# Kernel optimization log

Hardware: AMD Instinct MI355X
Metric: run time of the kernel (lower is better)

## Reference

```python
import jax, jax.numpy as jnp
import numpy as np

N_CLASSES = 91  # classes 0..90; class 0 (background) is excluded from the mean


def setup_inputs() -> dict:
    key = jax.random.key(0)
    k1, k2 = jax.random.split(key)
    B, H, W = 64, 512, 512
    # label maps with integer class ids in [0, 91); `inputs` stored as float32
    # to mirror the original (compared elementwise against integer i)
    inputs = jax.random.randint(k1, (B, H, W), 0, N_CLASSES).astype(jnp.float32)
    targets = jax.random.randint(k2, (B, H, W), 0, N_CLASSES).astype(jnp.int32)
    return {"inputs": inputs, "targets": targets, "smooth": 1}


def reference(inputs, targets, smooth):
    # Single-pass histogram formulation of the original per-class loop:
    #   intersection_i = #{p : inputs[p]==i and targets[p]==i}
    #   total_i        = #{inputs==i} + #{targets==i}
    #   union_i        = total_i - intersection_i
    n = N_CLASSES
    inp = inputs.reshape(-1).astype(jnp.int32)
    tgt = targets.reshape(-1).astype(jnp.int32)
    cnt_in = jnp.bincount(inp, length=n).astype(jnp.float32)
    cnt_tg = jnp.bincount(tgt, length=n).astype(jnp.float32)
    # positions where prediction == target contribute to that class's intersection;
    # mismatches are routed to a dummy bin n and dropped
    inter = jnp.bincount(jnp.where(inp == tgt, inp, n), length=n + 1)[:n].astype(jnp.float32)
    union = cnt_in + cnt_tg - inter
    smooth_f = jnp.float32(smooth)
    iou = (inter[1:] + smooth_f) / (union[1:] + smooth_f)  # classes 1..n-1
    return jnp.sum(iou) / (n - 1)
```

## Files before the change

### kernel.cpp

```cpp
#include <hip/hip_runtime.h>

#define NCLS 91
#define NPPAD 8284
#define NHIST (3 * NCLS)
#define BS 256
#define NBLK 1024
#define U 8
#define NCHUNK 2

__global__ __launch_bounds__(BS) void miou_hist(const float* __restrict__ inp,
                                                const int* __restrict__ tgt,
                                                unsigned int* __restrict__ ws,
                                                int n4) {
    __shared__ unsigned int ph[NPPAD];
    uint4* z = (uint4*)ph;
    for (int i = threadIdx.x; i < NPPAD / 4; i += BS) z[i] = make_uint4(0u, 0u, 0u, 0u);
    __syncthreads();

    const float4* in4 = (const float4*)inp;
    const int4* tg4 = (const int4*)tgt;
    const int stride = NBLK * BS;
    const int i0 = blockIdx.x * BS + threadIdx.x;

    if (i0 + (NCHUNK * U - 1) * stride < n4) {
        #pragma unroll
        for (int c = 0; c < NCHUNK; ++c) {
            const int base = i0 + c * U * stride;
            float4 f[U];
            int4 t[U];
            #pragma unroll
            for (int u = 0; u < U; ++u) {
                f[u] = in4[base + u * stride];
                t[u] = tg4[base + u * stride];
            }
            __builtin_amdgcn_sched_barrier(0);
            #pragma unroll
            for (int u = 0; u < U; ++u) {
                atomicAdd(&ph[(int)f[u].x * NCLS + t[u].x], 1u);
                atomicAdd(&ph[(int)f[u].y * NCLS + t[u].y], 1u);
                atomicAdd(&ph[(int)f[u].z * NCLS + t[u].z], 1u);
                atomicAdd(&ph[(int)f[u].w * NCLS + t[u].w], 1u);
            }
        }
    } else {
        for (int i = i0; i < n4; i += stride) {
            float4 f = in4[i];
            int4 t = tg4[i];
            atomicAdd(&ph[(int)f.x * NCLS + t.x], 1u);
            atomicAdd(&ph[(int)f.y * NCLS + t.y], 1u);
            atomicAdd(&ph[(int)f.z * NCLS + t.z], 1u);
            atomicAdd(&ph[(int)f.w * NCLS + t.w], 1u);
        }
    }
    __syncthreads();

    int t = threadIdx.x;
    if (t < NCLS) {
        const unsigned int* p = ph + t * NCLS;
        unsigned int s0 = 0, s1 = 0, s2 = 0, s3 = 0;
        int k = 0;
        for (; k + 3 < NCLS; k += 4) { s0 += p[k]; s1 += p[k+1]; s2 += p[k+2]; s3 += p[k+3]; }
        for (; k < NCLS; ++k) s0 += p[k];
        unsigned int s = s0 + s1 + s2 + s3;
        if (s) atomicAdd(&ws[t], s);
        unsigned int d = p[t];
        if (d) atomicAdd(&ws[2 * NCLS + t], d);
    } else if (t >= 128 && t < 128 + NCLS) {
        int c = t - 128;
        unsigned int s0 = 0, s1 = 0, s2 = 0, s3 = 0;
        int a = 0;
        for (; a + 3 < NCLS; a += 4) {
            s0 += ph[a * NCLS + c];
            s1 += ph[(a + 1) * NCLS + c];
            s2 += ph[(a + 2) * NCLS + c];
            s3 += ph[(a + 3) * NCLS + c];
        }
        for (; a < NCLS; ++a) s0 += ph[a * NCLS + c];
        unsigned int s = s0 + s1 + s2 + s3;
        if (s) atomicAdd(&ws[NCLS + c], s);
    }
}

__global__ void miou_tail(const float* __restrict__ inp, const int* __restrict__ tgt,
                          unsigned int* __restrict__ ws, int e0, int n) {
    int i = e0 + blockIdx.x * 256 + threadIdx.x;
    if (i < n) {
        int a = (int)inp[i];
        int t = tgt[i];
        atomicAdd(&ws[a], 1u);
        atomicAdd(&ws[NCLS + t], 1u);
        if (a == t) atomicAdd(&ws[2 * NCLS + a], 1u);
    }
}

__global__ void miou_finalize(const unsigned int* __restrict__ ws,
                              const int* __restrict__ smooth_p,
                              float* __restrict__ out) {
    int lane = threadIdx.x;
    float s = (float)(*smooth_p);
    float acc = 0.f;
    for (int c = 1 + lane; c < NCLS; c += 64) {
        float ci = (float)ws[c];
        float ct = (float)ws[NCLS + c];
        float it = (float)ws[2 * NCLS + c];
        float un = ci + ct - it;
        acc += (it + s) / (un + s);
    }
    #pragma unroll
    for (int off = 32; off; off >>= 1) acc += __shfl_down(acc, off);
    if (lane == 0) out[0] = acc / (float)(NCLS - 1);
}

extern "C" void kernel_launch(void* const* d_in, const int* in_sizes, int n_in,
                              void* d_out, int out_size, void* d_ws, size_t ws_size,
                              hipStream_t stream) {
    const float* inp = (const float*)d_in[0];
    const int* tgt = (const int*)d_in[1];
    const int* smooth_p = (const int*)d_in[2];
    float* out = (float*)d_out;
    unsigned int* ws = (unsigned int*)d_ws;

    int n = in_sizes[0];
    int n4 = n >> 2;
    int e0 = n & ~3;

    hipMemsetAsync(ws, 0, NHIST * sizeof(unsigned int), stream);
    miou_hist<<<NBLK, BS, 0, stream>>>(inp, tgt, ws, n4);
    if (e0 < n)
        miou_tail<<<(n - e0 + 255) / 256, 256, 0, stream>>>(inp, tgt, ws, e0, n);
    miou_finalize<<<1, 64, 0, stream>>>(ws, smooth_p, out);
}
```

Baseline: 159.4 us.

## Software-pipeline histogram loads with inline asm and per-wave contiguous tiles

Replaces the grid-strided load pattern with per-wavefront contiguous tiles and inline-asm global loads. Two register sets are double-buffered, with explicit vmcnt waits, so the next batch of loads is in flight while the LDS atomics for the current batch run. The fast path is specialised to exactly the test problem size (64x512x512), and a generic fallback kernel handles any other size. The handwritten asm and manual waitcnt bypass compiler scheduling and could be fragile.

Measured after the change: 157.4 us. No clear change (-1.3%).

```diff
diff --git a/kernel.cpp b/kernel.cpp
--- a/kernel.cpp
+++ b/kernel.cpp
@@ -5,53 +5,82 @@
 #define NHIST (3 * NCLS)
 #define BS 256
 #define NBLK 1024
-#define U 8
-#define NCHUNK 2
+
+typedef float __attribute__((ext_vector_type(4))) f32x4;
+typedef int   __attribute__((ext_vector_type(4))) i32x4;
+
+__device__ __forceinline__ void issue8(const f32x4* pf0, const f32x4* pf1,
+                                       const f32x4* pf2, const f32x4* pf3,
+                                       const i32x4* pt0, const i32x4* pt1,
+                                       const i32x4* pt2, const i32x4* pt3,
+                                       f32x4& F0, f32x4& F1, f32x4& F2, f32x4& F3,
+                                       i32x4& T0, i32x4& T1, i32x4& T2, i32x4& T3) {
+    asm volatile(
+        "global_load_dwordx4 %0, %8, off\n\t"
+        "global_load_dwordx4 %1, %9, off\n\t"
+        "global_load_dwordx4 %2, %10, off\n\t"
+        "global_load_dwordx4 %3, %11, off\n\t"
+        "global_load_dwordx4 %4, %12, off\n\t"
+        "global_load_dwordx4 %5, %13, off\n\t"
+        "global_load_dwordx4 %6, %14, off\n\t"
+        "global_load_dwordx4 %7, %15, off"
+        : "=&v"(F0), "=&v"(F1), "=&v"(F2), "=&v"(F3),
+          "=&v"(T0), "=&v"(T1), "=&v"(T2), "=&v"(T3)
+        : "v"(pf0), "v"(pf1), "v"(pf2), "v"(pf3),
+          "v"(pt0), "v"(pt1), "v"(pt2), "v"(pt3)
+        : "memory");
+}
+
+__device__ __forceinline__ void proc16(unsigned int* __restrict__ ph,
+                                       f32x4 F0, f32x4 F1, f32x4 F2, f32x4 F3,
+                                       i32x4 T0, i32x4 T1, i32x4 T2, i32x4 T3) {
+#define P1(F, T, c) atomicAdd(&ph[(int)F[c] * NCLS + T[c]], 1u)
+#define P4(F, T) P1(F, T, 0); P1(F, T, 1); P1(F, T, 2); P1(F, T, 3)
+    P4(F0, T0); P4(F1, T1); P4(F2, T2); P4(F3, T3);
+#undef P4
+#undef P1
+}
+
+#define WAITV(N)                                            \
+    asm volatile("s_waitcnt vmcnt(" #N ")" ::: "memory");   \
+    __builtin_amdgcn_sched_barrier(0)
 
 __global__ __launch_bounds__(BS) void miou_hist(const float* __restrict__ inp,
                                                 const int* __restrict__ tgt,
-                                                unsigned int* __restrict__ ws,
-                                                int n4) {
+                                                unsigned int* __restrict__ ws) {
     __shared__ unsigned int ph[NPPAD];
     uint4* z = (uint4*)ph;
     for (int i = threadIdx.x; i < NPPAD / 4; i += BS) z[i] = make_uint4(0u, 0u, 0u, 0u);
     __syncthreads();
 
-    const float4* in4 = (const float4*)inp;
-    const int4* tg4 = (const int4*)tgt;
-    const int stride = NBLK * BS;
-    const int i0 = blockIdx.x * BS + threadIdx.x;
+    const int W = blockIdx.x * 4 + (threadIdx.x >> 6);
+    const int lane = threadIdx.x & 63;
+    const f32x4* fb = (const f32x4*)inp;
+    const i32x4* tb = (const i32x4*)tgt;
+#define PF(g, u) (fb + (((W * 4 + (g)) * 4 + (u)) * 64 + lane))
+#define PT(g, u) (tb + (((W * 4 + (g)) * 4 + (u)) * 64 + lane))
 
-    if (i0 + (NCHUNK * U - 1) * stride < n4) {
-        #pragma unroll
-        for (int c = 0; c < NCHUNK; ++c) {
-            const int base = i0 + c * U * stride;
-            float4 f[U];
-            int4 t[U];
-            #pragma unroll
-            for (int u = 0; u < U; ++u) {
-                f[u] = in4[base + u * stride];
-                t[u] = tg4[base + u * stride];
-            }
-            __builtin_amdgcn_sched_barrier(0);
-            #pragma unroll
-            for (int u = 0; u < U; ++u) {
-                atomicAdd(&ph[(int)f[u].x * NCLS + t[u].x], 1u);
-                atomicAdd(&ph[(int)f[u].y * NCLS + t[u].y], 1u);
-                atomicAdd(&ph[(int)f[u].z * NCLS + t[u].z], 1u);
-                atomicAdd(&ph[(int)f[u].w * NCLS + t[u].w], 1u);
-            }
-        }
-    } else {
-        for (int i = i0; i < n4; i += stride) {
-            float4 f = in4[i];
-            int4 t = tg4[i];
-            atomicAdd(&ph[(int)f.x * NCLS + t.x], 1u);
-            atomicAdd(&ph[(int)f.y * NCLS + t.y], 1u);
-            atomicAdd(&ph[(int)f.z * NCLS + t.z], 1u);
-            atomicAdd(&ph[(int)f.w * NCLS + t.w], 1u);
-        }
-    }
+    f32x4 A0, A1, A2, A3, B0, B1, B2, B3;
+    i32x4 A4, A5, A6, A7, B4, B5, B6, B7;
+
+    issue8(PF(0,0), PF(0,1), PF(0,2), PF(0,3), PT(0,0), PT(0,1), PT(0,2), PT(0,3),
+           A0, A1, A2, A3, A4, A5, A6, A7);
+    issue8(PF(1,0), PF(1,1), PF(1,2), PF(1,3), PT(1,0), PT(1,1), PT(1,2), PT(1,3),
+           B0, B1, B2, B3, B4, B5, B6, B7);
+    WAITV(8);
+    proc16(ph, A0, A1, A2, A3, A4, A5, A6, A7);
+    issue8(PF(2,0), PF(2,1), PF(2,2), PF(2,3), PT(2,0), PT(2,1), PT(2,2), PT(2,3),
+           A0, A1, A2, A3, A4, A5, A6, A7);
+    WAITV(8);
+    proc16(ph, B0, B1, B2, B3, B4, B5, B6, B7);
+    issue8(PF(3,0), PF(3,1), PF(3,2), PF(3,3), PT(3,0), PT(3,1), PT(3,2), PT(3,3),
+           B0, B1, B2, B3, B4, B5, B6, B7);
+    WAITV(8);
+    proc16(ph, A0, A1, A2, A3, A4, A5, A6, A7);
+    WAITV(0);
+    proc16(ph, B0, B1, B2, B3, B4, B5, B6, B7);
+#undef PF
+#undef PT
     __syncthreads();
 
     int t = threadIdx.x;
@@ -81,15 +110,34 @@
     }
 }
 
-__global__ void miou_tail(const float* __restrict__ inp, const int* __restrict__ tgt,
-                          unsigned int* __restrict__ ws, int e0, int n) {
-    int i = e0 + blockIdx.x * 256 + threadIdx.x;
-    if (i < n) {
+__global__ __launch_bounds__(BS) void miou_hist_generic(const float* __restrict__ inp,
+                                                        const int* __restrict__ tgt,
+                                                        unsigned int* __restrict__ ws,
+                                                        int n) {
+    __shared__ unsigned int ph[NPPAD];
+    uint4* z = (uint4*)ph;
+    for (int i = threadIdx.x; i < NPPAD / 4; i += BS) z[i] = make_uint4(0u, 0u, 0u, 0u);
+    __syncthreads();
+    int stride = gridDim.x * BS;
+    for (int i = blockIdx.x * BS + threadIdx.x; i < n; i += stride) {
         int a = (int)inp[i];
         int t = tgt[i];
-        atomicAdd(&ws[a], 1u);
-        atomicAdd(&ws[NCLS + t], 1u);
-        if (a == t) atomicAdd(&ws[2 * NCLS + a], 1u);
+        atomicAdd(&ph[a * NCLS + t], 1u);
+    }
+    __syncthreads();
+    int t = threadIdx.x;
+    if (t < NCLS) {
+        const unsigned int* p = ph + t * NCLS;
+        unsigned int s = 0;
+        for (int k = 0; k < NCLS; ++k) s += p[k];
+        if (s) atomicAdd(&ws[t], s);
+        unsigned int d = p[t];
+        if (d) atomicAdd(&ws[2 * NCLS + t], d);
+    } else if (t >= 128 && t < 128 + NCLS) {
+        int c = t - 128;
+        unsigned int s = 0;
+        for (int a = 0; a < NCLS; ++a) s += ph[a * NCLS + c];
+        if (s) atomicAdd(&ws[NCLS + c], s);
     }
 }
 
@@ -121,12 +169,11 @@
     unsigned int* ws = (unsigned int*)d_ws;
 
     int n = in_sizes[0];
-    int n4 = n >> 2;
-    int e0 = n & ~3;
-
     hipMemsetAsync(ws, 0, NHIST * sizeof(unsigned int), stream);
-    miou_hist<<<NBLK, BS, 0, stream>>>(inp, tgt, ws, n4);
-    if (e0 < n)
-        miou_tail<<<(n - e0 + 255) / 256, 256, 0, stream>>>(inp, tgt, ws, e0, n);
+    if (n == NBLK * 4 * 4 * 4 * 64 * 4) {
+        miou_hist<<<NBLK, BS, 0, stream>>>(inp, tgt, ws);
+    } else {
+        miou_hist_generic<<<1024, BS, 0, stream>>>(inp, tgt, ws, n);
+    }
     miou_finalize<<<1, 64, 0, stream>>>(ws, smooth_p, out);
 }
```
